# Performance work log

Measured on AMD Instinct MI355X. Metric: run time of the kernel, lower is better.

The kernel has to match this reference:

```python
import jax, jax.numpy as jnp
import numpy as np


def fwht(x):
    """Unnormalized fast Walsh-Hadamard transform over a 1-D vector (len = power of 2).
    Matches the torch chunk/cat stage ordering (MSB-first butterfly)."""
    n = x.shape[0]
    ll = int(round(np.log2(n)))
    for ii in range(ll):
        x = x.reshape(2 ** ii, 2, -1)
        x = jnp.concatenate([x[:, :1] + x[:, 1:], x[:, :1] - x[:, 1:]], axis=1)
    return x.reshape(n)


@jax.custom_vjp
def fwht_ff(x):
    # mirrors torch FastWalshHadamard.apply: plain FWHT forward,
    # backward = FWHT(grad) / sqrt(n) (as defined in the original autograd Function)
    return fwht(x)

def _fwht_ff_fwd(x):
    scale = jnp.asarray(1.0 / np.sqrt(float(x.shape[0])), x.dtype)
    return fwht(x), scale

def _fwht_ff_bwd(scale, g):
    return (scale * fwht(g),)

fwht_ff.defvjp(_fwht_ff_fwd, _fwht_ff_bwd)


def fastfood(theta, BB, Pi, GG, DD):
    """Fastfood projection of theta (dim dd) to DD dims using fixed vars."""
    LL = BB.shape[0]
    dd = theta.shape[0]
    k = min(dd, LL)  # F.pad with negative pad truncates; replicate that
    xx = jnp.zeros(LL, theta.dtype).at[:k].set(theta[:k])
    m2 = fwht(BB * xx)          # H B x
    m4 = m2[Pi] * GG            # G Pi H B x
    m5 = fwht_ff(m4)            # H G Pi H B x
    divisor = jnp.sqrt(LL * jnp.sum(GG * GG))
    return m5[:DD] / (divisor * np.sqrt(float(DD) / LL))


def _mk_ff_vars(key, DD):
    ll = int(np.ceil(np.log2(DD)))
    LL = 2 ** ll
    k1, k2, k3 = jax.random.split(key, 3)
    BB = jax.random.randint(k1, (LL,), 0, 2).astype(jnp.float32) * 2.0 - 1.0
    Pi = jax.random.permutation(k2, LL).astype(jnp.int32)
    GG = jax.random.normal(k3, (LL,), dtype=jnp.float32)
    return BB, Pi, GG


D_IN, D_HID, D_OUT = 768, 3072, 768
INTRINSIC = 2048
BATCH = 256


def setup_inputs() -> dict:
    key = jax.random.key(0)
    ks = jax.random.split(key, 12)
    x = jax.random.normal(ks[0], (BATCH, D_IN), dtype=jnp.float32)
    # original initializes intrinsic_parameter to zeros; use small randn so the
    # Fastfood path contributes non-trivially to the output for testing
    theta = jax.random.normal(ks[1], (INTRINSIC,), dtype=jnp.float32) * 0.01
    init_W1 = jax.random.normal(ks[2], (D_HID, D_IN), dtype=jnp.float32) * 0.02
    init_b1 = jax.random.normal(ks[3], (D_HID,), dtype=jnp.float32) * 0.02
    init_W2 = jax.random.normal(ks[4], (D_OUT, D_HID), dtype=jnp.float32) * 0.02
    init_b2 = jax.random.normal(ks[5], (D_OUT,), dtype=jnp.float32) * 0.02
    BB_W1, Pi_W1, GG_W1 = _mk_ff_vars(ks[6], D_HID * D_IN)
    BB_b1, Pi_b1, GG_b1 = _mk_ff_vars(ks[7], D_HID)
    BB_W2, Pi_W2, GG_W2 = _mk_ff_vars(ks[8], D_OUT * D_HID)
    BB_b2, Pi_b2, GG_b2 = _mk_ff_vars(ks[9], D_OUT)
    return {
        'x': x, 'theta': theta,
        'init_W1': init_W1, 'init_b1': init_b1, 'init_W2': init_W2, 'init_b2': init_b2,
        'BB_W1': BB_W1, 'Pi_W1': Pi_W1, 'GG_W1': GG_W1,
        'BB_b1': BB_b1, 'Pi_b1': Pi_b1, 'GG_b1': GG_b1,
        'BB_W2': BB_W2, 'Pi_W2': Pi_W2, 'GG_W2': GG_W2,
        'BB_b2': BB_b2, 'Pi_b2': Pi_b2, 'GG_b2': GG_b2,
    }


def reference(x, theta, init_W1, init_b1, init_W2, init_b2,
              BB_W1, Pi_W1, GG_W1, BB_b1, Pi_b1, GG_b1,
              BB_W2, Pi_W2, GG_W2, BB_b2, Pi_b2, GG_b2):
    # param = initial_value + fastfood(theta) for every wrapped parameter
    W1 = init_W1 + fastfood(theta, BB_W1, Pi_W1, GG_W1, init_W1.size).reshape(init_W1.shape)
    b1 = init_b1 + fastfood(theta, BB_b1, Pi_b1, GG_b1, init_b1.size)
    W2 = init_W2 + fastfood(theta, BB_W2, Pi_W2, GG_W2, init_W2.size).reshape(init_W2.shape)
    b2 = init_b2 + fastfood(theta, BB_b2, Pi_b2, GG_b2, init_b2.size)
    # wrapped module forward: Linear -> ReLU -> Linear
    h = jax.nn.relu(x @ W1.T + b1)
    return h @ W2.T + b2
```

## Files before the change

### kernel.cpp

```cpp
#include <hip/hip_runtime.h>
#include <hip/hip_bf16.h>

typedef __attribute__((ext_vector_type(8))) short bf16x8;
typedef __attribute__((ext_vector_type(8))) unsigned short u16x8;
typedef __attribute__((ext_vector_type(4))) float f32x4;

template <int N, int S>
__device__ __forceinline__ void reg_fwht(float* v) {
#pragma unroll
  for (int h = 1; h < N; h <<= 1)
#pragma unroll
    for (int g = 0; g < N; g += 2 * h)
#pragma unroll
      for (int j = 0; j < h; ++j) {
        float a = v[(g + j) * S], b = v[(g + j + h) * S];
        v[(g + j) * S] = a + b;
        v[(g + j + h) * S] = a - b;
      }
}

__device__ __forceinline__ unsigned short f2bf(float f) {
  unsigned u = __float_as_uint(f);
  unsigned r = (u + 0x7fff + ((u >> 16) & 1)) >> 16;
  return (unsigned short)r;
}

__device__ __forceinline__ void lds_fwht(float* s, int n, int tid, int T) {
  for (int h = 1; h < n; h <<= 1) {
    __syncthreads();
    for (int t = tid; t < (n >> 1); t += T) {
      int i0 = ((t & ~(h - 1)) << 1) | (t & (h - 1));
      int i1 = i0 + h;
      float a = s[i0], b = s[i1];
      s[i0] = a + b;
      s[i1] = a - b;
    }
  }
  __syncthreads();
}

__device__ __forceinline__ void fwht2048_block(float w[8], float* pad,
                                               float* dst, int t) {
  reg_fwht<8, 1>(w);
#pragma unroll
  for (int j = 0; j < 8; ++j) {
    int i = t + 256 * j;
    pad[i + 4 * (i >> 5)] = w[j];
  }
  __syncthreads();
  {
    int base = 8 * t + 4 * (t >> 2);
    float4 a = *(float4*)(pad + base);
    float4 b = *(float4*)(pad + base + 4);
    float u[8] = {a.x, a.y, a.z, a.w, b.x, b.y, b.z, b.w};
    reg_fwht<8, 1>(u);
    *(float4*)(pad + base) = make_float4(u[0], u[1], u[2], u[3]);
    *(float4*)(pad + base + 4) = make_float4(u[4], u[5], u[6], u[7]);
  }
  __syncthreads();
  {
    int b0 = (t & 7) + 64 * (t >> 3);
    float u[8];
#pragma unroll
    for (int j = 0; j < 8; ++j) {
      int i = b0 + 8 * j;
      u[j] = pad[i + 4 * (i >> 5)];
    }
    reg_fwht<8, 1>(u);
#pragma unroll
    for (int j = 0; j < 8; ++j) {
      int i = b0 + 8 * j;
      pad[i + 4 * (i >> 5)] = u[j];
    }
  }
  __syncthreads();
#pragma unroll
  for (int g = 0; g < 2; ++g) {
    int b0 = (t & 63) + 256 * ((g << 2) | (t >> 6));
    float u[4];
#pragma unroll
    for (int j = 0; j < 4; ++j) {
      int i = b0 + 64 * j;
      u[j] = pad[i + 4 * (i >> 5)];
    }
    reg_fwht<4, 1>(u);
#pragma unroll
    for (int j = 0; j < 4; ++j) dst[b0 + 64 * j] = u[j];
  }
  __syncthreads();
}

__global__ __launch_bounds__(256) void k_pre(
    const float* __restrict__ theta, const float* __restrict__ BB0,
    const float* __restrict__ BB1, float* __restrict__ m2s,
    const float* __restrict__ x, __hip_bfloat16* __restrict__ xb) {
  __shared__ __align__(16) float pad[2304];
  int b = blockIdx.x, t = threadIdx.x;
  if (b < 2) {
    const float* BB = b ? BB1 : BB0;
    float w[8];
#pragma unroll
    for (int j = 0; j < 8; ++j) {
      int i = t + 256 * j;
      w[j] = BB[i] * theta[i];
    }
    fwht2048_block(w, pad, m2s + b * 2048, t);
  } else {
    int id0 = (b - 2) * 256 + t;
#pragma unroll
    for (int it = 0; it < 2; ++it) {
      int id = id0 + it * 24576;
      float4 xv = ((const float4*)x)[id];
      ushort4 o;
      o.x = f2bf(xv.x);
      o.y = f2bf(xv.y);
      o.z = f2bf(xv.z);
      o.w = f2bf(xv.w);
      ((ushort4*)xb)[id] = o;
    }
  }
}

#define LLW 4194304

__global__ __launch_bounds__(256) void k_front(
    const int* __restrict__ Pi1, const float* __restrict__ GG1,
    const int* __restrict__ Pi2, const float* __restrict__ GG2,
    const float* __restrict__ m2s, unsigned short* __restrict__ m4b,
    float* __restrict__ partial, const float* __restrict__ theta,
    const float* __restrict__ BBb1, const int* __restrict__ Pib1,
    const float* __restrict__ GGb1, const float* __restrict__ ib1,
    float* __restrict__ b1w, const float* __restrict__ BBb2,
    const int* __restrict__ Pib2, const float* __restrict__ GGb2,
    const float* __restrict__ ib2, float* __restrict__ b2w) {
  __shared__ __align__(16) float s[9216];
  __shared__ float red[4];
  int b = blockIdx.x, t = threadIdx.x;

  if (b >= 2) {
    int bb = b - 2;
    int pipe = bb >> 9, chunk = bb & 511;
    const int* Pi = pipe ? Pi2 : Pi1;
    const float* GG = pipe ? GG2 : GG1;
    const float* mm = m2s + pipe * 2048;
    for (int u = t; u < 512; u += 256) ((float4*)s)[u] = ((const float4*)mm)[u];
    __syncthreads();

    long base = (long)chunk * 8192;
    const int4* p4 = (const int4*)(Pi + base);
    const float4* g4 = (const float4*)(GG + base);
    float v[32];
    float lsum = 0.f;
#pragma unroll
    for (int j = 0; j < 8; ++j) {
      int4 p = p4[t + j * 256];
      float4 g = g4[t + j * 256];
      lsum += g.x * g.x + g.y * g.y + g.z * g.z + g.w * g.w;
      v[j * 4 + 0] = s[p.x & 2047] * g.x;
      v[j * 4 + 1] = s[p.y & 2047] * g.y;
      v[j * 4 + 2] = s[p.z & 2047] * g.z;
      v[j * 4 + 3] = s[p.w & 2047] * g.w;
    }
    for (int off = 32; off; off >>= 1) lsum += __shfl_down(lsum, off, 64);
    if ((t & 63) == 0) red[t >> 6] = lsum;

#pragma unroll
    for (int e = 0; e < 4; ++e) reg_fwht<8, 4>(v + e);

    __syncthreads();
    if (t == 0) partial[pipe * 512 + chunk] = red[0] + red[1] + red[2] + red[3];

#pragma unroll
    for (int j = 0; j < 8; ++j) {
      int A = t * 4 + 4 * (t >> 3) + j * 1152;
      *(float4*)(s + A) =
          make_float4(v[j * 4], v[j * 4 + 1], v[j * 4 + 2], v[j * 4 + 3]);
    }
    __syncthreads();
    {
      int b0 = (t & 31) + (t >> 5) * 1024;
      float w[32];
#pragma unroll
      for (int j2 = 0; j2 < 32; ++j2) {
        int i = b0 + j2 * 32;
        w[j2] = s[i + 4 * (i >> 5)];
      }
      reg_fwht<32, 1>(w);
#pragma unroll
      for (int j2 = 0; j2 < 32; ++j2) {
        int i = b0 + j2 * 32;
        s[i + 4 * (i >> 5)] = w[j2];
      }
    }
    __syncthreads();
#pragma unroll
    for (int q = 0; q < 8; ++q) {
      float4 r = *(const float4*)(s + t * 36 + q * 4);
      v[q * 4 + 0] = r.x;
      v[q * 4 + 1] = r.y;
      v[q * 4 + 2] = r.z;
      v[q * 4 + 3] = r.w;
    }
    reg_fwht<32, 1>(v);
    unsigned short* o = m4b + (long)pipe * LLW;
    long a0 = (long)(2 * t) * 8192 + (long)chunk * 16;
#pragma unroll
    for (int q = 0; q < 4; ++q) {
      u16x8 pk;
#pragma unroll
      for (int e = 0; e < 8; ++e) pk[e] = f2bf(v[q * 8 + e]);
      *(u16x8*)(o + a0 + (q >> 1) * 8192 + (q & 1) * 8) = pk;
    }
  } else if (b == 0) {
    float* tabd = s + 6144;
    float w[8];
#pragma unroll
    for (int j = 0; j < 8; ++j) {
      int i = t + 256 * j;
      w[j] = BBb1[i] * theta[i];
    }
    fwht2048_block(w, s, tabd, t);

    float w16[16];
    float lsum = 0.f;
#pragma unroll
    for (int j = 0; j < 16; ++j) {
      int i = t + 256 * j;
      float g = GGb1[i];
      lsum += g * g;
      w16[j] = tabd[Pib1[i] & 2047] * g;
    }
    reg_fwht<16, 1>(w16);
#pragma unroll
    for (int j = 0; j < 16; ++j) {
      int i = t + 256 * j;
      s[i + 4 * (i >> 5)] = w16[j];
    }
    for (int off = 32; off; off >>= 1) lsum += __shfl_down(lsum, off, 64);
    if ((t & 63) == 0) s[4608 + (t >> 6)] = lsum;
    __syncthreads();
    float S = s[4608] + s[4609] + s[4610] + s[4611];
    {
      int base16 = 16 * t + 4 * (t >> 1);
      float u[16];
#pragma unroll
      for (int q = 0; q < 4; ++q) {
        float4 r = *(float4*)(s + base16 + q * 4);
        u[q * 4 + 0] = r.x;
        u[q * 4 + 1] = r.y;
        u[q * 4 + 2] = r.z;
        u[q * 4 + 3] = r.w;
      }
      reg_fwht<16, 1>(u);
#pragma unroll
      for (int q = 0; q < 4; ++q)
        *(float4*)(s + base16 + q * 4) =
            make_float4(u[q * 4], u[q * 4 + 1], u[q * 4 + 2], u[q * 4 + 3]);
    }
    __syncthreads();
    {
      float scale = 1.0f / sqrtf(S * 3072.0f);
      int b0 = (t & 15) + 256 * (t >> 4);
      float u[16];
#pragma unroll
      for (int j = 0; j < 16; ++j) {
        int i = b0 + 16 * j;
        u[j] = s[i + 4 * (i >> 5)];
      }
      reg_fwht<16, 1>(u);
#pragma unroll
      for (int j = 0; j < 16; ++j) {
        int i = b0 + 16 * j;
        if (i < 3072) b1w[i] = ib1[i] + u[j] * scale;
      }
    }
  } else {
    float* tab2 = s;
    float* m42 = s + 1024;
    for (int i = t; i < 1024; i += 256) tab2[i] = BBb2[i] * theta[i];
    lds_fwht(tab2, 1024, t, 256);
    float lsum = 0.f;
    for (int i = t; i < 1024; i += 256) {
      float g = GGb2[i];
      lsum += g * g;
      m42[i] = tab2[Pib2[i] & 1023] * g;
    }
    for (int off = 32; off; off >>= 1) lsum += __shfl_down(lsum, off, 64);
    if ((t & 63) == 0) s[2048 + (t >> 6)] = lsum;
    lds_fwht(m42, 1024, t, 256);
    float S = s[2048] + s[2049] + s[2050] + s[2051];
    float scale = 1.0f / sqrtf(S * 768.0f);
    for (int i = t; i < 768; i += 256) b2w[i] = ib2[i] + m42[i] * scale;
  }
}

__global__ __launch_bounds__(256) void k_f2c(
    const unsigned short* __restrict__ m4b, const float* __restrict__ iW1,
    const float* __restrict__ iW2, const float* __restrict__ partial,
    __hip_bfloat16* __restrict__ W1b, __hip_bfloat16* __restrict__ W2b) {
  __shared__ __align__(16) float s[10480];
  __shared__ float red[4];
  int b = blockIdx.x, t = threadIdx.x;
  int pipe = b >> 9;
  int lb = b & 511;
  int g = ((lb & 7) << 6) | (lb >> 3);
  int l0 = g * 16;
  const unsigned short* mp = m4b + (long)pipe * LLW + (long)g * 8192;
  const float* initW = pipe ? iW2 : iW1;
  unsigned short* outW = (unsigned short*)(pipe ? W2b : W1b);

  {
    float ps = partial[pipe * 512 + t] + partial[pipe * 512 + 256 + t];
    for (int off = 32; off; off >>= 1) ps += __shfl_down(ps, off, 64);
    if ((t & 63) == 0) red[t >> 6] = ps;
  }

#pragma unroll
  for (int q = 0; q < 4; ++q) {
    u16x8 raw = *(const u16x8*)(mp + t * 32 + q * 8);
    int r = 2 * t + (q >> 1), cb = (q & 1) * 8;
    float* dp = s + r * 20 + (r >> 5) * 16 + cb;
    float4 f0, f1v;
    f0.x = __uint_as_float((unsigned)raw[0] << 16);
    f0.y = __uint_as_float((unsigned)raw[1] << 16);
    f0.z = __uint_as_float((unsigned)raw[2] << 16);
    f0.w = __uint_as_float((unsigned)raw[3] << 16);
    f1v.x = __uint_as_float((unsigned)raw[4] << 16);
    f1v.y = __uint_as_float((unsigned)raw[5] << 16);
    f1v.z = __uint_as_float((unsigned)raw[6] << 16);
    f1v.w = __uint_as_float((unsigned)raw[7] << 16);
    *(float4*)dp = f0;
    *(float4*)(dp + 4) = f1v;
  }
  __syncthreads();

  {
    int c = t & 15, rg = t >> 4;
    float w[32];
#pragma unroll
    for (int j = 0; j < 32; ++j) {
      int r = rg * 32 + j;
      w[j] = s[r * 20 + (r >> 5) * 16 + c];
    }
    reg_fwht<32, 1>(w);
#pragma unroll
    for (int j = 0; j < 32; ++j) {
      int r = rg * 32 + j;
      s[r * 20 + (r >> 5) * 16 + c] = w[j];
    }
  }
  __syncthreads();

  {
    int c = t & 15;
    float w[32];
#pragma unroll
    for (int k = 0; k < 2; ++k) {
      int b0 = (t >> 4) * 2 + k;
#pragma unroll
      for (int j4 = 0; j4 < 16; ++j4) {
        int r = b0 + 32 * j4;
        w[k * 16 + j4] = s[r * 20 + (r >> 5) * 16 + c];
      }
      reg_fwht<16, 1>(w + k * 16);
#pragma unroll
      for (int j4 = 0; j4 < 16; ++j4) {
        int r = b0 + 32 * j4;
        s[r * 20 + (r >> 5) * 16 + c] = w[k * 16 + j4];
      }
    }
  }
  __syncthreads();

  float S = red[0] + red[1] + red[2] + red[3];
  float scale = 1.0f / sqrtf(S * 2359296.0f);
#pragma unroll
  for (int u = 0; u < 5; ++u) {
    int idx = t + u * 256;
    if (idx < 1152) {
      int r = idx >> 2, c4 = (idx & 3) * 4;
      const float* sp = s + r * 20 + (r >> 5) * 16 + c4;
      long gi = (long)r * 8192 + l0 + c4;
      float4 iv = *(const float4*)(initW + gi);
      ushort4 pk;
      pk.x = f2bf(iv.x + sp[0] * scale);
      pk.y = f2bf(iv.y + sp[1] * scale);
      pk.z = f2bf(iv.z + sp[2] * scale);
      pk.w = f2bf(iv.w + sp[3] * scale);
      *(ushort4*)(outW + gi) = pk;
    }
  }
}

template <int NACC, int SPLITK, bool RELU, bool OUT_BF16>
__global__ __launch_bounds__(256) void k_gemm(
    const __hip_bfloat16* __restrict__ A, const __hip_bfloat16* __restrict__ B,
    const float* __restrict__ bias, void* __restrict__ C, int M, int N, int K) {
  __shared__ float red[4 * NACC * 320];
  int wave = threadIdx.x >> 6, lane = threadIdx.x & 63;
  int tileid = blockIdx.x * (4 / SPLITK) + wave / SPLITK;
  int sk = wave % SPLITK;
  int ntiles = N / (16 * NACC);
  int mt = tileid / ntiles, nt = tileid % ntiles;
  int ml = lane & 15;
  int q = lane >> 4;
  const short* As = (const short*)A;
  const short* Bs = (const short*)B;
  long arow = (long)(mt * 16 + ml) * K + q * 8;
  int KS = K / SPLITK, k0 = sk * KS;
  f32x4 acc[NACC] = {};
  for (int k = k0; k < k0 + KS; k += 32) {
    bf16x8 av = *(const bf16x8*)(As + arow + k);
#pragma unroll
    for (int a = 0; a < NACC; ++a) {
      int n = nt * 16 * NACC + a * 16 + ml;
      bf16x8 bv = *(const bf16x8*)(Bs + (long)n * K + q * 8 + k);
      acc[a] = __builtin_amdgcn_mfma_f32_16x16x32_bf16(av, bv, acc[a], 0, 0, 0);
    }
  }
#pragma unroll
  for (int a = 0; a < NACC; ++a)
#pragma unroll
    for (int r = 0; r < 4; ++r)
      red[(wave * NACC + a) * 320 + lane * 5 + r] = acc[a][r];
  __syncthreads();
  if (sk == 0) {
#pragma unroll
    for (int a = 0; a < NACC; ++a) {
      int n = nt * 16 * NACC + a * 16 + ml;
      float bv = bias[n];
#pragma unroll
      for (int r = 0; r < 4; ++r) {
        float vv = bv;
#pragma unroll
        for (int j = 0; j < SPLITK; ++j)
          vv += red[((wave + j) * NACC + a) * 320 + lane * 5 + r];
        int mm = mt * 16 + q * 4 + r;
        if (RELU) vv = fmaxf(vv, 0.f);
        if (OUT_BF16)
          ((__hip_bfloat16*)C)[(long)mm * N + n] = __float2bfloat16(vv);
        else
          ((float*)C)[(long)mm * N + n] = vv;
      }
    }
  }
}

#define OFF_PART 0
#define OFF_M2S 4096
#define OFF_M4B (OFF_M2S + 16384)
#define OFF_W1B (OFF_M4B + 2 * LLW * 2)
#define OFF_W2B (OFF_W1B + 4718592)
#define OFF_HB (OFF_W2B + 4718592)
#define OFF_XB (OFF_HB + 1572864)
#define OFF_B1 (OFF_XB + 393216)
#define OFF_B2 (OFF_B1 + 12288)

extern "C" void kernel_launch(void* const* d_in, const int* in_sizes, int n_in,
                              void* d_out, int out_size, void* d_ws,
                              size_t ws_size, hipStream_t stream) {
  const float* x = (const float*)d_in[0];
  const float* theta = (const float*)d_in[1];
  const float* iW1 = (const float*)d_in[2];
  const float* ib1 = (const float*)d_in[3];
  const float* iW2 = (const float*)d_in[4];
  const float* ib2 = (const float*)d_in[5];
  const float* BB_W1 = (const float*)d_in[6];
  const int* Pi_W1 = (const int*)d_in[7];
  const float* GG_W1 = (const float*)d_in[8];
  const float* BB_b1 = (const float*)d_in[9];
  const int* Pi_b1 = (const int*)d_in[10];
  const float* GG_b1 = (const float*)d_in[11];
  const float* BB_W2 = (const float*)d_in[12];
  const int* Pi_W2 = (const int*)d_in[13];
  const float* GG_W2 = (const float*)d_in[14];
  const float* BB_b2 = (const float*)d_in[15];
  const int* Pi_b2 = (const int*)d_in[16];
  const float* GG_b2 = (const float*)d_in[17];

  char* ws = (char*)d_ws;
  float* partial = (float*)(ws + OFF_PART);
  float* m2s = (float*)(ws + OFF_M2S);
  unsigned short* m4b = (unsigned short*)(ws + OFF_M4B);
  __hip_bfloat16* W1b = (__hip_bfloat16*)(ws + OFF_W1B);
  __hip_bfloat16* W2b = (__hip_bfloat16*)(ws + OFF_W2B);
  __hip_bfloat16* hb = (__hip_bfloat16*)(ws + OFF_HB);
  __hip_bfloat16* xb = (__hip_bfloat16*)(ws + OFF_XB);
  float* b1w = (float*)(ws + OFF_B1);
  float* b2w = (float*)(ws + OFF_B2);

  k_pre<<<98, 256, 0, stream>>>(theta, BB_W1, BB_W2, m2s, x, xb);
  k_front<<<1026, 256, 0, stream>>>(Pi_W1, GG_W1, Pi_W2, GG_W2, m2s, m4b,
                                    partial, theta, BB_b1, Pi_b1, GG_b1, ib1,
                                    b1w, BB_b2, Pi_b2, GG_b2, ib2, b2w);
  k_f2c<<<1024, 256, 0, stream>>>(m4b, iW1, iW2, partial, W1b, W2b);
  k_gemm<2, 2, true, true><<<768, 256, 0, stream>>>(xb, W1b, b1w, hb, 256,
                                                    3072, 768);
  k_gemm<1, 4, false, false><<<768, 256, 0, stream>>>(hb, W2b, b2w, d_out, 256,
                                                      768, 3072);
}
```

Measured before the change: 217.8 us.

## Fuse prelude into front kernel and overlap W2 conversion with first GEMM

Each front block now recomputes the 2048-point H·B·theta transform itself instead of reading it from a separate pre-kernel, and the x→bf16 conversion moves into extra blocks of the same launch. The f2c kernel is split so W1 is built first, then a mixed kernel runs the W2 conversion alongside the first GEMM. This removes one launch and one global round trip and lets memory-bound and MFMA work share the GPU. The cost is redundant FWHT work in all 1024 blocks and possible load imbalance between heterogeneous blocks. The mixed kernel also uses the 10480-float f2c shared array for the GEMM reduction buffer.

```diff
diff --git a/kernel.cpp b/kernel.cpp
--- a/kernel.cpp
+++ b/kernel.cpp
@@ -90,23 +90,187 @@
   __syncthreads();
 }
 
-__global__ __launch_bounds__(256) void k_pre(
-    const float* __restrict__ theta, const float* __restrict__ BB0,
-    const float* __restrict__ BB1, float* __restrict__ m2s,
-    const float* __restrict__ x, __hip_bfloat16* __restrict__ xb) {
-  __shared__ __align__(16) float pad[2304];
+#define LLW 4194304
+
+__global__ __launch_bounds__(256) void k_front(
+    const float* __restrict__ BB1, const int* __restrict__ Pi1,
+    const float* __restrict__ GG1, const float* __restrict__ BB2,
+    const int* __restrict__ Pi2, const float* __restrict__ GG2,
+    unsigned short* __restrict__ m4b, float* __restrict__ partial,
+    const float* __restrict__ theta, const float* __restrict__ BBb1,
+    const int* __restrict__ Pib1, const float* __restrict__ GGb1,
+    const float* __restrict__ ib1, float* __restrict__ b1w,
+    const float* __restrict__ BBb2, const int* __restrict__ Pib2,
+    const float* __restrict__ GGb2, const float* __restrict__ ib2,
+    float* __restrict__ b2w, const float* __restrict__ x,
+    __hip_bfloat16* __restrict__ xb) {
+  __shared__ __align__(16) float s[9216];
+  __shared__ float red[4];
   int b = blockIdx.x, t = threadIdx.x;
-  if (b < 2) {
-    const float* BB = b ? BB1 : BB0;
+
+  if (b < 1024) {
+    int pipe = b >> 9, chunk = b & 511;
+    const float* BB = pipe ? BB2 : BB1;
+    const int* Pi = pipe ? Pi2 : Pi1;
+    const float* GG = pipe ? GG2 : GG1;
+
+    {
+      float w8[8];
+#pragma unroll
+      for (int j = 0; j < 8; ++j) {
+        int i = t + 256 * j;
+        w8[j] = BB[i] * theta[i];
+      }
+      fwht2048_block(w8, s + 2304, s, t);
+    }
+
+    long base = (long)chunk * 8192;
+    const int4* p4 = (const int4*)(Pi + base);
+    const float4* g4 = (const float4*)(GG + base);
+    float v[32];
+    float lsum = 0.f;
+#pragma unroll
+    for (int j = 0; j < 8; ++j) {
+      int4 p = p4[t + j * 256];
+      float4 g = g4[t + j * 256];
+      lsum += g.x * g.x + g.y * g.y + g.z * g.z + g.w * g.w;
+      v[j * 4 + 0] = s[p.x & 2047] * g.x;
+      v[j * 4 + 1] = s[p.y & 2047] * g.y;
+      v[j * 4 + 2] = s[p.z & 2047] * g.z;
+      v[j * 4 + 3] = s[p.w & 2047] * g.w;
+    }
+    for (int off = 32; off; off >>= 1) lsum += __shfl_down(lsum, off, 64);
+    if ((t & 63) == 0) red[t >> 6] = lsum;
+
+#pragma unroll
+    for (int e = 0; e < 4; ++e) reg_fwht<8, 4>(v + e);
+
+    __syncthreads();
+    if (t == 0) partial[pipe * 512 + chunk] = red[0] + red[1] + red[2] + red[3];
+
+#pragma unroll
+    for (int j = 0; j < 8; ++j) {
+      int A = t * 4 + 4 * (t >> 3) + j * 1152;
+      *(float4*)(s + A) =
+          make_float4(v[j * 4], v[j * 4 + 1], v[j * 4 + 2], v[j * 4 + 3]);
+    }
+    __syncthreads();
+    {
+      int b0 = (t & 31) + (t >> 5) * 1024;
+      float w[32];
+#pragma unroll
+      for (int j2 = 0; j2 < 32; ++j2) {
+        int i = b0 + j2 * 32;
+        w[j2] = s[i + 4 * (i >> 5)];
+      }
+      reg_fwht<32, 1>(w);
+#pragma unroll
+      for (int j2 = 0; j2 < 32; ++j2) {
+        int i = b0 + j2 * 32;
+        s[i + 4 * (i >> 5)] = w[j2];
+      }
+    }
+    __syncthreads();
+#pragma unroll
+    for (int q = 0; q < 8; ++q) {
+      float4 r = *(const float4*)(s + t * 36 + q * 4);
+      v[q * 4 + 0] = r.x;
+      v[q * 4 + 1] = r.y;
+      v[q * 4 + 2] = r.z;
+      v[q * 4 + 3] = r.w;
+    }
+    reg_fwht<32, 1>(v);
+    unsigned short* o = m4b + (long)pipe * LLW;
+    long a0 = (long)(2 * t) * 8192 + (long)chunk * 16;
+#pragma unroll
+    for (int q = 0; q < 4; ++q) {
+      u16x8 pk;
+#pragma unroll
+      for (int e = 0; e < 8; ++e) pk[e] = f2bf(v[q * 8 + e]);
+      *(u16x8*)(o + a0 + (q >> 1) * 8192 + (q & 1) * 8) = pk;
+    }
+  } else if (b == 1024) {
+    float* tabd = s + 6144;
     float w[8];
 #pragma unroll
     for (int j = 0; j < 8; ++j) {
       int i = t + 256 * j;
-      w[j] = BB[i] * theta[i];
-    }
-    fwht2048_block(w, pad, m2s + b * 2048, t);
+      w[j] = BBb1[i] * theta[i];
+    }
+    fwht2048_block(w, s, tabd, t);
+
+    float w16[16];
+    float lsum = 0.f;
+#pragma unroll
+    for (int j = 0; j < 16; ++j) {
+      int i = t + 256 * j;
+      float g = GGb1[i];
+      lsum += g * g;
+      w16[j] = tabd[Pib1[i] & 2047] * g;
+    }
+    reg_fwht<16, 1>(w16);
+#pragma unroll
+    for (int j = 0; j < 16; ++j) {
+      int i = t + 256 * j;
+      s[i + 4 * (i >> 5)] = w16[j];
+    }
+    for (int off = 32; off; off >>= 1) lsum += __shfl_down(lsum, off, 64);
+    if ((t & 63) == 0) s[4608 + (t >> 6)] = lsum;
+    __syncthreads();
+    float S = s[4608] + s[4609] + s[4610] + s[4611];
+    {
+      int base16 = 16 * t + 4 * (t >> 1);
+      float u[16];
+#pragma unroll
+      for (int q = 0; q < 4; ++q) {
+        float4 r = *(float4*)(s + base16 + q * 4);
+        u[q * 4 + 0] = r.x;
+        u[q * 4 + 1] = r.y;
+        u[q * 4 + 2] = r.z;
+        u[q * 4 + 3] = r.w;
+      }
+      reg_fwht<16, 1>(u);
+#pragma unroll
+      for (int q = 0; q < 4; ++q)
+        *(float4*)(s + base16 + q * 4) =
+            make_float4(u[q * 4], u[q * 4 + 1], u[q * 4 + 2], u[q * 4 + 3]);
+    }
+    __syncthreads();
+    {
+      float scale = 1.0f / sqrtf(S * 3072.0f);
+      int b0 = (t & 15) + 256 * (t >> 4);
+      float u[16];
+#pragma unroll
+      for (int j = 0; j < 16; ++j) {
+        int i = b0 + 16 * j;
+        u[j] = s[i + 4 * (i >> 5)];
+      }
+      reg_fwht<16, 1>(u);
+#pragma unroll
+      for (int j = 0; j < 16; ++j) {
+        int i = b0 + 16 * j;
+        if (i < 3072) b1w[i] = ib1[i] + u[j] * scale;
+      }
+    }
+  } else if (b == 1025) {
+    float* tab2 = s;
+    float* m42 = s + 1024;
+    for (int i = t; i < 1024; i += 256) tab2[i] = BBb2[i] * theta[i];
+    lds_fwht(tab2, 1024, t, 256);
+    float lsum = 0.f;
+    for (int i = t; i < 1024; i += 256) {
+      float g = GGb2[i];
+      lsum += g * g;
+      m42[i] = tab2[Pib2[i] & 1023] * g;
+    }
+    for (int off = 32; off; off >>= 1) lsum += __shfl_down(lsum, off, 64);
+    if ((t & 63) == 0) s[2048 + (t >> 6)] = lsum;
+    lds_fwht(m42, 1024, t, 256);
+    float S = s[2048] + s[2049] + s[2050] + s[2051];
+    float scale = 1.0f / sqrtf(S * 768.0f);
+    for (int i = t; i < 768; i += 256) b2w[i] = ib2[i] + m42[i] * scale;
   } else {
-    int id0 = (b - 2) * 256 + t;
+    int id0 = (b - 1026) * 256 + t;
 #pragma unroll
     for (int it = 0; it < 2; ++it) {
       int id = id0 + it * 24576;
@@ -121,196 +285,17 @@
   }
 }
 
-#define LLW 4194304
-
-__global__ __launch_bounds__(256) void k_front(
-    const int* __restrict__ Pi1, const float* __restrict__ GG1,
-    const int* __restrict__ Pi2, const float* __restrict__ GG2,
-    const float* __restrict__ m2s, unsigned short* __restrict__ m4b,
-    float* __restrict__ partial, const float* __restrict__ theta,
-    const float* __restrict__ BBb1, const int* __restrict__ Pib1,
-    const float* __restrict__ GGb1, const float* __restrict__ ib1,
-    float* __restrict__ b1w, const float* __restrict__ BBb2,
-    const int* __restrict__ Pib2, const float* __restrict__ GGb2,
-    const float* __restrict__ ib2, float* __restrict__ b2w) {
-  __shared__ __align__(16) float s[9216];
-  __shared__ float red[4];
-  int b = blockIdx.x, t = threadIdx.x;
-
-  if (b >= 2) {
-    int bb = b - 2;
-    int pipe = bb >> 9, chunk = bb & 511;
-    const int* Pi = pipe ? Pi2 : Pi1;
-    const float* GG = pipe ? GG2 : GG1;
-    const float* mm = m2s + pipe * 2048;
-    for (int u = t; u < 512; u += 256) ((float4*)s)[u] = ((const float4*)mm)[u];
-    __syncthreads();
-
-    long base = (long)chunk * 8192;
-    const int4* p4 = (const int4*)(Pi + base);
-    const float4* g4 = (const float4*)(GG + base);
-    float v[32];
-    float lsum = 0.f;
-#pragma unroll
-    for (int j = 0; j < 8; ++j) {
-      int4 p = p4[t + j * 256];
-      float4 g = g4[t + j * 256];
-      lsum += g.x * g.x + g.y * g.y + g.z * g.z + g.w * g.w;
-      v[j * 4 + 0] = s[p.x & 2047] * g.x;
-      v[j * 4 + 1] = s[p.y & 2047] * g.y;
-      v[j * 4 + 2] = s[p.z & 2047] * g.z;
-      v[j * 4 + 3] = s[p.w & 2047] * g.w;
-    }
-    for (int off = 32; off; off >>= 1) lsum += __shfl_down(lsum, off, 64);
-    if ((t & 63) == 0) red[t >> 6] = lsum;
-
-#pragma unroll
-    for (int e = 0; e < 4; ++e) reg_fwht<8, 4>(v + e);
-
-    __syncthreads();
-    if (t == 0) partial[pipe * 512 + chunk] = red[0] + red[1] + red[2] + red[3];
-
-#pragma unroll
-    for (int j = 0; j < 8; ++j) {
-      int A = t * 4 + 4 * (t >> 3) + j * 1152;
-      *(float4*)(s + A) =
-          make_float4(v[j * 4], v[j * 4 + 1], v[j * 4 + 2], v[j * 4 + 3]);
-    }
-    __syncthreads();
-    {
-      int b0 = (t & 31) + (t >> 5) * 1024;
-      float w[32];
-#pragma unroll
-      for (int j2 = 0; j2 < 32; ++j2) {
-        int i = b0 + j2 * 32;
-        w[j2] = s[i + 4 * (i >> 5)];
-      }
-      reg_fwht<32, 1>(w);
-#pragma unroll
-      for (int j2 = 0; j2 < 32; ++j2) {
-        int i = b0 + j2 * 32;
-        s[i + 4 * (i >> 5)] = w[j2];
-      }
-    }
-    __syncthreads();
-#pragma unroll
-    for (int q = 0; q < 8; ++q) {
-      float4 r = *(const float4*)(s + t * 36 + q * 4);
-      v[q * 4 + 0] = r.x;
-      v[q * 4 + 1] = r.y;
-      v[q * 4 + 2] = r.z;
-      v[q * 4 + 3] = r.w;
-    }
-    reg_fwht<32, 1>(v);
-    unsigned short* o = m4b + (long)pipe * LLW;
-    long a0 = (long)(2 * t) * 8192 + (long)chunk * 16;
-#pragma unroll
-    for (int q = 0; q < 4; ++q) {
-      u16x8 pk;
-#pragma unroll
-      for (int e = 0; e < 8; ++e) pk[e] = f2bf(v[q * 8 + e]);
-      *(u16x8*)(o + a0 + (q >> 1) * 8192 + (q & 1) * 8) = pk;
-    }
-  } else if (b == 0) {
-    float* tabd = s + 6144;
-    float w[8];
-#pragma unroll
-    for (int j = 0; j < 8; ++j) {
-      int i = t + 256 * j;
-      w[j] = BBb1[i] * theta[i];
-    }
-    fwht2048_block(w, s, tabd, t);
-
-    float w16[16];
-    float lsum = 0.f;
-#pragma unroll
-    for (int j = 0; j < 16; ++j) {
-      int i = t + 256 * j;
-      float g = GGb1[i];
-      lsum += g * g;
-      w16[j] = tabd[Pib1[i] & 2047] * g;
-    }
-    reg_fwht<16, 1>(w16);
-#pragma unroll
-    for (int j = 0; j < 16; ++j) {
-      int i = t + 256 * j;
-      s[i + 4 * (i >> 5)] = w16[j];
-    }
-    for (int off = 32; off; off >>= 1) lsum += __shfl_down(lsum, off, 64);
-    if ((t & 63) == 0) s[4608 + (t >> 6)] = lsum;
-    __syncthreads();
-    float S = s[4608] + s[4609] + s[4610] + s[4611];
-    {
-      int base16 = 16 * t + 4 * (t >> 1);
-      float u[16];
-#pragma unroll
-      for (int q = 0; q < 4; ++q) {
-        float4 r = *(float4*)(s + base16 + q * 4);
-        u[q * 4 + 0] = r.x;
-        u[q * 4 + 1] = r.y;
-        u[q * 4 + 2] = r.z;
-        u[q * 4 + 3] = r.w;
-      }
-      reg_fwht<16, 1>(u);
-#pragma unroll
-      for (int q = 0; q < 4; ++q)
-        *(float4*)(s + base16 + q * 4) =
-            make_float4(u[q * 4], u[q * 4 + 1], u[q * 4 + 2], u[q * 4 + 3]);
-    }
-    __syncthreads();
-    {
-      float scale = 1.0f / sqrtf(S * 3072.0f);
-      int b0 = (t & 15) + 256 * (t >> 4);
-      float u[16];
-#pragma unroll
-      for (int j = 0; j < 16; ++j) {
-        int i = b0 + 16 * j;
-        u[j] = s[i + 4 * (i >> 5)];
-      }
-      reg_fwht<16, 1>(u);
-#pragma unroll
-      for (int j = 0; j < 16; ++j) {
-        int i = b0 + 16 * j;
-        if (i < 3072) b1w[i] = ib1[i] + u[j] * scale;
-      }
-    }
-  } else {
-    float* tab2 = s;
-    float* m42 = s + 1024;
-    for (int i = t; i < 1024; i += 256) tab2[i] = BBb2[i] * theta[i];
-    lds_fwht(tab2, 1024, t, 256);
-    float lsum = 0.f;
-    for (int i = t; i < 1024; i += 256) {
-      float g = GGb2[i];
-      lsum += g * g;
-      m42[i] = tab2[Pib2[i] & 1023] * g;
-    }
-    for (int off = 32; off; off >>= 1) lsum += __shfl_down(lsum, off, 64);
-    if ((t & 63) == 0) s[2048 + (t >> 6)] = lsum;
-    lds_fwht(m42, 1024, t, 256);
-    float S = s[2048] + s[2049] + s[2050] + s[2051];
-    float scale = 1.0f / sqrtf(S * 768.0f);
-    for (int i = t; i < 768; i += 256) b2w[i] = ib2[i] + m42[i] * scale;
-  }
-}
-
-__global__ __launch_bounds__(256) void k_f2c(
-    const unsigned short* __restrict__ m4b, const float* __restrict__ iW1,
-    const float* __restrict__ iW2, const float* __restrict__ partial,
-    __hip_bfloat16* __restrict__ W1b, __hip_bfloat16* __restrict__ W2b) {
-  __shared__ __align__(16) float s[10480];
-  __shared__ float red[4];
-  int b = blockIdx.x, t = threadIdx.x;
-  int pipe = b >> 9;
-  int lb = b & 511;
+__device__ __forceinline__ void f2c_body(const unsigned short* __restrict__ mpipe,
+                                         const float* __restrict__ initW,
+                                         unsigned short* __restrict__ outW,
+                                         const float* __restrict__ partial_p,
+                                         int lb, int t, float* s, float* red) {
   int g = ((lb & 7) << 6) | (lb >> 3);
   int l0 = g * 16;
-  const unsigned short* mp = m4b + (long)pipe * LLW + (long)g * 8192;
-  const float* initW = pipe ? iW2 : iW1;
-  unsigned short* outW = (unsigned short*)(pipe ? W2b : W1b);
+  const unsigned short* mp = mpipe + (long)g * 8192;
 
   {
-    float ps = partial[pipe * 512 + t] + partial[pipe * 512 + 256 + t];
+    float ps = partial_p[t] + partial_p[256 + t];
     for (int off = 32; off; off >>= 1) ps += __shfl_down(ps, off, 64);
     if ((t & 63) == 0) red[t >> 6] = ps;
   }
@@ -393,12 +378,12 @@
 }
 
 template <int NACC, int SPLITK, bool RELU, bool OUT_BF16>
-__global__ __launch_bounds__(256) void k_gemm(
+__device__ __forceinline__ void gemm_body(
     const __hip_bfloat16* __restrict__ A, const __hip_bfloat16* __restrict__ B,
-    const float* __restrict__ bias, void* __restrict__ C, int M, int N, int K) {
-  __shared__ float red[4 * NACC * 320];
-  int wave = threadIdx.x >> 6, lane = threadIdx.x & 63;
-  int tileid = blockIdx.x * (4 / SPLITK) + wave / SPLITK;
+    const float* __restrict__ bias, void* __restrict__ C, int M, int N, int K,
+    int bid, int tid, float* red) {
+  int wave = tid >> 6, lane = tid & 63;
+  int tileid = bid * (4 / SPLITK) + wave / SPLITK;
   int sk = wave % SPLITK;
   int ntiles = N / (16 * NACC);
   int mt = tileid / ntiles, nt = tileid % ntiles;
@@ -444,6 +429,41 @@
       }
     }
   }
+}
+
+__global__ __launch_bounds__(256) void k_f2c_a(
+    const unsigned short* __restrict__ m4b, const float* __restrict__ iW1,
+    const float* __restrict__ partial, __hip_bfloat16* __restrict__ W1b) {
+  __shared__ __align__(16) float s[10480];
+  __shared__ float red[4];
+  f2c_body(m4b, iW1, (unsigned short*)W1b, partial, blockIdx.x, threadIdx.x, s,
+           red);
+}
+
+__global__ __launch_bounds__(256) void k_mix(
+    const unsigned short* __restrict__ m4b, const float* __restrict__ iW2,
+    const float* __restrict__ partial, __hip_bfloat16* __restrict__ W2b,
+    const __hip_bfloat16* __restrict__ xb, const __hip_bfloat16* __restrict__ W1b,
+    const float* __restrict__ b1w, __hip_bfloat16* __restrict__ hb) {
+  __shared__ __align__(16) float s[10480];
+  __shared__ float red[4];
+  int b = blockIdx.x, t = threadIdx.x;
+  if (b < 512) {
+    f2c_body(m4b + (long)LLW, iW2, (unsigned short*)W2b, partial + 512, b, t,
+             s, red);
+  } else {
+    gemm_body<2, 2, true, true>(xb, W1b, b1w, hb, 256, 3072, 768, b - 512, t,
+                                s);
+  }
+}
+
+template <int NACC, int SPLITK, bool RELU, bool OUT_BF16>
+__global__ __launch_bounds__(256) void k_gemm(
+    const __hip_bfloat16* __restrict__ A, const __hip_bfloat16* __restrict__ B,
+    const float* __restrict__ bias, void* __restrict__ C, int M, int N, int K) {
+  __shared__ float red[4 * NACC * 320];
+  gemm_body<NACC, SPLITK, RELU, OUT_BF16>(A, B, bias, C, M, N, K, blockIdx.x,
+                                          threadIdx.x, red);
 }
 
 #define OFF_PART 0
@@ -480,7 +500,6 @@
 
   char* ws = (char*)d_ws;
   float* partial = (float*)(ws + OFF_PART);
-  float* m2s = (float*)(ws + OFF_M2S);
   unsigned short* m4b = (unsigned short*)(ws + OFF_M4B);
   __hip_bfloat16* W1b = (__hip_bfloat16*)(ws + OFF_W1B);
   __hip_bfloat16* W2b = (__hip_bfloat16*)(ws + OFF_W2B);
@@ -489,13 +508,12 @@
   float* b1w = (float*)(ws + OFF_B1);
   float* b2w = (float*)(ws + OFF_B2);
 
-  k_pre<<<98, 256, 0, stream>>>(theta, BB_W1, BB_W2, m2s, x, xb);
-  k_front<<<1026, 256, 0, stream>>>(Pi_W1, GG_W1, Pi_W2, GG_W2, m2s, m4b,
-                                    partial, theta, BB_b1, Pi_b1, GG_b1, ib1,
-                                    b1w, BB_b2, Pi_b2, GG_b2, ib2, b2w);
-  k_f2c<<<1024, 256, 0, stream>>>(m4b, iW1, iW2, partial, W1b, W2b);
-  k_gemm<2, 2, true, true><<<768, 256, 0, stream>>>(xb, W1b, b1w, hb, 256,
-                                                    3072, 768);
+  k_front<<<1122, 256, 0, stream>>>(BB_W1, Pi_W1, GG_W1, BB_W2, Pi_W2, GG_W2,
+                                    m4b, partial, theta, BB_b1, Pi_b1, GG_b1,
+                                    ib1, b1w, BB_b2, Pi_b2, GG_b2, ib2, b2w, x,
+                                    xb);
+  k_f2c_a<<<512, 256, 0, stream>>>(m4b, iW1, partial, W1b);
+  k_mix<<<1280, 256, 0, stream>>>(m4b, iW2, partial, W2b, xb, W1b, b1w, hb);
   k_gemm<1, 4, false, false><<<768, 256, 0, stream>>>(hb, W2b, b2w, d_out, 256,
                                                       768, 3072);
 }
```

After: 218.1 us. No clear change (+0.1%).

## Fuse pre-FWHT into front kernel and enlarge GEMM tiles

Applied to the files above, without the earlier changes.

Removes the separate k_pre launch by having each of the 1024 chunk blocks redundantly compute the 2048-point H·B·theta transform in shared memory, and moves the x-to-bf16 conversion into extra blocks of k_front. This drops one kernel launch and the m2s round trip through global memory, at the cost of repeating the small FWHT in every block. The GEMM template parameters are also doubled so each block does more work and half as many blocks are launched.

```diff
diff --git a/kernel.cpp b/kernel.cpp
--- a/kernel.cpp
+++ b/kernel.cpp
@@ -4,6 +4,8 @@
 typedef __attribute__((ext_vector_type(8))) short bf16x8;
 typedef __attribute__((ext_vector_type(8))) unsigned short u16x8;
 typedef __attribute__((ext_vector_type(4))) float f32x4;
+
+#define LLW 4194304
 
 template <int N, int S>
 __device__ __forceinline__ void reg_fwht(float* v) {
@@ -90,23 +92,186 @@
   __syncthreads();
 }
 
-__global__ __launch_bounds__(256) void k_pre(
-    const float* __restrict__ theta, const float* __restrict__ BB0,
-    const float* __restrict__ BB1, float* __restrict__ m2s,
-    const float* __restrict__ x, __hip_bfloat16* __restrict__ xb) {
-  __shared__ __align__(16) float pad[2304];
+__global__ __launch_bounds__(256) void k_front(
+    const float* __restrict__ BB1, const int* __restrict__ Pi1,
+    const float* __restrict__ GG1, const float* __restrict__ BB2,
+    const int* __restrict__ Pi2, const float* __restrict__ GG2,
+    unsigned short* __restrict__ m4b, float* __restrict__ partial,
+    const float* __restrict__ theta, const float* __restrict__ BBb1,
+    const int* __restrict__ Pib1, const float* __restrict__ GGb1,
+    const float* __restrict__ ib1, float* __restrict__ b1w,
+    const float* __restrict__ BBb2, const int* __restrict__ Pib2,
+    const float* __restrict__ GGb2, const float* __restrict__ ib2,
+    float* __restrict__ b2w, const float* __restrict__ x,
+    __hip_bfloat16* __restrict__ xb) {
+  __shared__ __align__(16) float s[9216];
+  __shared__ float red[4];
   int b = blockIdx.x, t = threadIdx.x;
-  if (b < 2) {
-    const float* BB = b ? BB1 : BB0;
+
+  if (b >= 2 && b < 1026) {
+    int bb = b - 2;
+    int pipe = bb >> 9, chunk = bb & 511;
+    const float* BB = pipe ? BB2 : BB1;
+    const int* Pi = pipe ? Pi2 : Pi1;
+    const float* GG = pipe ? GG2 : GG1;
+
+    {
+      float w8[8];
+#pragma unroll
+      for (int j = 0; j < 8; ++j) {
+        int i = t + 256 * j;
+        w8[j] = BB[i] * theta[i];
+      }
+      fwht2048_block(w8, s + 2304, s, t);
+    }
+
+    long base = (long)chunk * 8192;
+    const int4* p4 = (const int4*)(Pi + base);
+    const float4* g4 = (const float4*)(GG + base);
+    float v[32];
+    float lsum = 0.f;
+#pragma unroll
+    for (int j = 0; j < 8; ++j) {
+      int4 pp = p4[t + j * 256];
+      float4 g = g4[t + j * 256];
+      lsum += g.x * g.x + g.y * g.y + g.z * g.z + g.w * g.w;
+      v[j * 4 + 0] = s[pp.x & 2047] * g.x;
+      v[j * 4 + 1] = s[pp.y & 2047] * g.y;
+      v[j * 4 + 2] = s[pp.z & 2047] * g.z;
+      v[j * 4 + 3] = s[pp.w & 2047] * g.w;
+    }
+    for (int off = 32; off; off >>= 1) lsum += __shfl_down(lsum, off, 64);
+    if ((t & 63) == 0) red[t >> 6] = lsum;
+
+#pragma unroll
+    for (int e = 0; e < 4; ++e) reg_fwht<8, 4>(v + e);
+
+    __syncthreads();
+    if (t == 0) partial[pipe * 512 + chunk] = red[0] + red[1] + red[2] + red[3];
+
+#pragma unroll
+    for (int j = 0; j < 8; ++j) {
+      int A = t * 4 + 4 * (t >> 3) + j * 1152;
+      *(float4*)(s + A) =
+          make_float4(v[j * 4], v[j * 4 + 1], v[j * 4 + 2], v[j * 4 + 3]);
+    }
+    __syncthreads();
+    {
+      int b0 = (t & 31) + (t >> 5) * 1024;
+      float w[32];
+#pragma unroll
+      for (int j2 = 0; j2 < 32; ++j2) {
+        int i = b0 + j2 * 32;
+        w[j2] = s[i + 4 * (i >> 5)];
+      }
+      reg_fwht<32, 1>(w);
+#pragma unroll
+      for (int j2 = 0; j2 < 32; ++j2) {
+        int i = b0 + j2 * 32;
+        s[i + 4 * (i >> 5)] = w[j2];
+      }
+    }
+    __syncthreads();
+#pragma unroll
+    for (int q = 0; q < 8; ++q) {
+      float4 r = *(const float4*)(s + t * 36 + q * 4);
+      v[q * 4 + 0] = r.x;
+      v[q * 4 + 1] = r.y;
+      v[q * 4 + 2] = r.z;
+      v[q * 4 + 3] = r.w;
+    }
+    reg_fwht<32, 1>(v);
+    unsigned short* o = m4b + (long)pipe * LLW;
+    long a0 = (long)(2 * t) * 8192 + (long)chunk * 16;
+#pragma unroll
+    for (int q = 0; q < 4; ++q) {
+      u16x8 pk;
+#pragma unroll
+      for (int e = 0; e < 8; ++e) pk[e] = f2bf(v[q * 8 + e]);
+      *(u16x8*)(o + a0 + (q >> 1) * 8192 + (q & 1) * 8) = pk;
+    }
+  } else if (b == 0) {
+    float* tabd = s + 6144;
     float w[8];
 #pragma unroll
     for (int j = 0; j < 8; ++j) {
       int i = t + 256 * j;
-      w[j] = BB[i] * theta[i];
-    }
-    fwht2048_block(w, pad, m2s + b * 2048, t);
+      w[j] = BBb1[i] * theta[i];
+    }
+    fwht2048_block(w, s, tabd, t);
+
+    float w16[16];
+    float lsum = 0.f;
+#pragma unroll
+    for (int j = 0; j < 16; ++j) {
+      int i = t + 256 * j;
+      float g = GGb1[i];
+      lsum += g * g;
+      w16[j] = tabd[Pib1[i] & 2047] * g;
+    }
+    reg_fwht<16, 1>(w16);
+#pragma unroll
+    for (int j = 0; j < 16; ++j) {
+      int i = t + 256 * j;
+      s[i + 4 * (i >> 5)] = w16[j];
+    }
+    for (int off = 32; off; off >>= 1) lsum += __shfl_down(lsum, off, 64);
+    if ((t & 63) == 0) s[4608 + (t >> 6)] = lsum;
+    __syncthreads();
+    float S = s[4608] + s[4609] + s[4610] + s[4611];
+    {
+      int base16 = 16 * t + 4 * (t >> 1);
+      float u[16];
+#pragma unroll
+      for (int q = 0; q < 4; ++q) {
+        float4 r = *(float4*)(s + base16 + q * 4);
+        u[q * 4 + 0] = r.x;
+        u[q * 4 + 1] = r.y;
+        u[q * 4 + 2] = r.z;
+        u[q * 4 + 3] = r.w;
+      }
+      reg_fwht<16, 1>(u);
+#pragma unroll
+      for (int q = 0; q < 4; ++q)
+        *(float4*)(s + base16 + q * 4) =
+            make_float4(u[q * 4], u[q * 4 + 1], u[q * 4 + 2], u[q * 4 + 3]);
+    }
+    __syncthreads();
+    {
+      float scale = 1.0f / sqrtf(S * 3072.0f);
+      int b0 = (t & 15) + 256 * (t >> 4);
+      float u[16];
+#pragma unroll
+      for (int j = 0; j < 16; ++j) {
+        int i = b0 + 16 * j;
+        u[j] = s[i + 4 * (i >> 5)];
+      }
+      reg_fwht<16, 1>(u);
+#pragma unroll
+      for (int j = 0; j < 16; ++j) {
+        int i = b0 + 16 * j;
+        if (i < 3072) b1w[i] = ib1[i] + u[j] * scale;
+      }
+    }
+  } else if (b == 1) {
+    float* tab2 = s;
+    float* m42 = s + 1024;
+    for (int i = t; i < 1024; i += 256) tab2[i] = BBb2[i] * theta[i];
+    lds_fwht(tab2, 1024, t, 256);
+    float lsum = 0.f;
+    for (int i = t; i < 1024; i += 256) {
+      float g = GGb2[i];
+      lsum += g * g;
+      m42[i] = tab2[Pib2[i] & 1023] * g;
+    }
+    for (int off = 32; off; off >>= 1) lsum += __shfl_down(lsum, off, 64);
+    if ((t & 63) == 0) s[2048 + (t >> 6)] = lsum;
+    lds_fwht(m42, 1024, t, 256);
+    float S = s[2048] + s[2049] + s[2050] + s[2051];
+    float scale = 1.0f / sqrtf(S * 768.0f);
+    for (int i = t; i < 768; i += 256) b2w[i] = ib2[i] + m42[i] * scale;
   } else {
-    int id0 = (b - 2) * 256 + t;
+    int id0 = (b - 1026) * 256 + t;
 #pragma unroll
     for (int it = 0; it < 2; ++it) {
       int id = id0 + it * 24576;
@@ -118,179 +283,6 @@
       o.w = f2bf(xv.w);
       ((ushort4*)xb)[id] = o;
     }
-  }
-}
-
-#define LLW 4194304
-
-__global__ __launch_bounds__(256) void k_front(
-    const int* __restrict__ Pi1, const float* __restrict__ GG1,
-    const int* __restrict__ Pi2, const float* __restrict__ GG2,
-    const float* __restrict__ m2s, unsigned short* __restrict__ m4b,
-    float* __restrict__ partial, const float* __restrict__ theta,
-    const float* __restrict__ BBb1, const int* __restrict__ Pib1,
-    const float* __restrict__ GGb1, const float* __restrict__ ib1,
-    float* __restrict__ b1w, const float* __restrict__ BBb2,
-    const int* __restrict__ Pib2, const float* __restrict__ GGb2,
-    const float* __restrict__ ib2, float* __restrict__ b2w) {
-  __shared__ __align__(16) float s[9216];
-  __shared__ float red[4];
-  int b = blockIdx.x, t = threadIdx.x;
-
-  if (b >= 2) {
-    int bb = b - 2;
-    int pipe = bb >> 9, chunk = bb & 511;
-    const int* Pi = pipe ? Pi2 : Pi1;
-    const float* GG = pipe ? GG2 : GG1;
-    const float* mm = m2s + pipe * 2048;
-    for (int u = t; u < 512; u += 256) ((float4*)s)[u] = ((const float4*)mm)[u];
-    __syncthreads();
-
-    long base = (long)chunk * 8192;
-    const int4* p4 = (const int4*)(Pi + base);
-    const float4* g4 = (const float4*)(GG + base);
-    float v[32];
-    float lsum = 0.f;
-#pragma unroll
-    for (int j = 0; j < 8; ++j) {
-      int4 p = p4[t + j * 256];
-      float4 g = g4[t + j * 256];
-      lsum += g.x * g.x + g.y * g.y + g.z * g.z + g.w * g.w;
-      v[j * 4 + 0] = s[p.x & 2047] * g.x;
-      v[j * 4 + 1] = s[p.y & 2047] * g.y;
-      v[j * 4 + 2] = s[p.z & 2047] * g.z;
-      v[j * 4 + 3] = s[p.w & 2047] * g.w;
-    }
-    for (int off = 32; off; off >>= 1) lsum += __shfl_down(lsum, off, 64);
-    if ((t & 63) == 0) red[t >> 6] = lsum;
-
-#pragma unroll
-    for (int e = 0; e < 4; ++e) reg_fwht<8, 4>(v + e);
-
-    __syncthreads();
-    if (t == 0) partial[pipe * 512 + chunk] = red[0] + red[1] + red[2] + red[3];
-
-#pragma unroll
-    for (int j = 0; j < 8; ++j) {
-      int A = t * 4 + 4 * (t >> 3) + j * 1152;
-      *(float4*)(s + A) =
-          make_float4(v[j * 4], v[j * 4 + 1], v[j * 4 + 2], v[j * 4 + 3]);
-    }
-    __syncthreads();
-    {
-      int b0 = (t & 31) + (t >> 5) * 1024;
-      float w[32];
-#pragma unroll
-      for (int j2 = 0; j2 < 32; ++j2) {
-        int i = b0 + j2 * 32;
-        w[j2] = s[i + 4 * (i >> 5)];
-      }
-      reg_fwht<32, 1>(w);
-#pragma unroll
-      for (int j2 = 0; j2 < 32; ++j2) {
-        int i = b0 + j2 * 32;
-        s[i + 4 * (i >> 5)] = w[j2];
-      }
-    }
-    __syncthreads();
-#pragma unroll
-    for (int q = 0; q < 8; ++q) {
-      float4 r = *(const float4*)(s + t * 36 + q * 4);
-      v[q * 4 + 0] = r.x;
-      v[q * 4 + 1] = r.y;
-      v[q * 4 + 2] = r.z;
-      v[q * 4 + 3] = r.w;
-    }
-    reg_fwht<32, 1>(v);
-    unsigned short* o = m4b + (long)pipe * LLW;
-    long a0 = (long)(2 * t) * 8192 + (long)chunk * 16;
-#pragma unroll
-    for (int q = 0; q < 4; ++q) {
-      u16x8 pk;
-#pragma unroll
-      for (int e = 0; e < 8; ++e) pk[e] = f2bf(v[q * 8 + e]);
-      *(u16x8*)(o + a0 + (q >> 1) * 8192 + (q & 1) * 8) = pk;
-    }
-  } else if (b == 0) {
-    float* tabd = s + 6144;
-    float w[8];
-#pragma unroll
-    for (int j = 0; j < 8; ++j) {
-      int i = t + 256 * j;
-      w[j] = BBb1[i] * theta[i];
-    }
-    fwht2048_block(w, s, tabd, t);
-
-    float w16[16];
-    float lsum = 0.f;
-#pragma unroll
-    for (int j = 0; j < 16; ++j) {
-      int i = t + 256 * j;
-      float g = GGb1[i];
-      lsum += g * g;
-      w16[j] = tabd[Pib1[i] & 2047] * g;
-    }
-    reg_fwht<16, 1>(w16);
-#pragma unroll
-    for (int j = 0; j < 16; ++j) {
-      int i = t + 256 * j;
-      s[i + 4 * (i >> 5)] = w16[j];
-    }
-    for (int off = 32; off; off >>= 1) lsum += __shfl_down(lsum, off, 64);
-    if ((t & 63) == 0) s[4608 + (t >> 6)] = lsum;
-    __syncthreads();
-    float S = s[4608] + s[4609] + s[4610] + s[4611];
-    {
-      int base16 = 16 * t + 4 * (t >> 1);
-      float u[16];
-#pragma unroll
-      for (int q = 0; q < 4; ++q) {
-        float4 r = *(float4*)(s + base16 + q * 4);
-        u[q * 4 + 0] = r.x;
-        u[q * 4 + 1] = r.y;
-        u[q * 4 + 2] = r.z;
-        u[q * 4 + 3] = r.w;
-      }
-      reg_fwht<16, 1>(u);
-#pragma unroll
-      for (int q = 0; q < 4; ++q)
-        *(float4*)(s + base16 + q * 4) =
-            make_float4(u[q * 4], u[q * 4 + 1], u[q * 4 + 2], u[q * 4 + 3]);
-    }
-    __syncthreads();
-    {
-      float scale = 1.0f / sqrtf(S * 3072.0f);
-      int b0 = (t & 15) + 256 * (t >> 4);
-      float u[16];
-#pragma unroll
-      for (int j = 0; j < 16; ++j) {
-        int i = b0 + 16 * j;
-        u[j] = s[i + 4 * (i >> 5)];
-      }
-      reg_fwht<16, 1>(u);
-#pragma unroll
-      for (int j = 0; j < 16; ++j) {
-        int i = b0 + 16 * j;
-        if (i < 3072) b1w[i] = ib1[i] + u[j] * scale;
-      }
-    }
-  } else {
-    float* tab2 = s;
-    float* m42 = s + 1024;
-    for (int i = t; i < 1024; i += 256) tab2[i] = BBb2[i] * theta[i];
-    lds_fwht(tab2, 1024, t, 256);
-    float lsum = 0.f;
-    for (int i = t; i < 1024; i += 256) {
-      float g = GGb2[i];
-      lsum += g * g;
-      m42[i] = tab2[Pib2[i] & 1023] * g;
-    }
-    for (int off = 32; off; off >>= 1) lsum += __shfl_down(lsum, off, 64);
-    if ((t & 63) == 0) s[2048 + (t >> 6)] = lsum;
-    lds_fwht(m42, 1024, t, 256);
-    float S = s[2048] + s[2049] + s[2050] + s[2051];
-    float scale = 1.0f / sqrtf(S * 768.0f);
-    for (int i = t; i < 768; i += 256) b2w[i] = ib2[i] + m42[i] * scale;
   }
 }
 
@@ -480,7 +472,6 @@
 
   char* ws = (char*)d_ws;
   float* partial = (float*)(ws + OFF_PART);
-  float* m2s = (float*)(ws + OFF_M2S);
   unsigned short* m4b = (unsigned short*)(ws + OFF_M4B);
   __hip_bfloat16* W1b = (__hip_bfloat16*)(ws + OFF_W1B);
   __hip_bfloat16* W2b = (__hip_bfloat16*)(ws + OFF_W2B);
@@ -489,13 +480,13 @@
   float* b1w = (float*)(ws + OFF_B1);
   float* b2w = (float*)(ws + OFF_B2);
 
-  k_pre<<<98, 256, 0, stream>>>(theta, BB_W1, BB_W2, m2s, x, xb);
-  k_front<<<1026, 256, 0, stream>>>(Pi_W1, GG_W1, Pi_W2, GG_W2, m2s, m4b,
-                                    partial, theta, BB_b1, Pi_b1, GG_b1, ib1,
-                                    b1w, BB_b2, Pi_b2, GG_b2, ib2, b2w);
+  k_front<<<1122, 256, 0, stream>>>(BB_W1, Pi_W1, GG_W1, BB_W2, Pi_W2, GG_W2,
+                                    m4b, partial, theta, BB_b1, Pi_b1, GG_b1,
+                                    ib1, b1w, BB_b2, Pi_b2, GG_b2, ib2, b2w, x,
+                                    xb);
   k_f2c<<<1024, 256, 0, stream>>>(m4b, iW1, iW2, partial, W1b, W2b);
-  k_gemm<2, 2, true, true><<<768, 256, 0, stream>>>(xb, W1b, b1w, hb, 256,
+  k_gemm<4, 2, true, true><<<384, 256, 0, stream>>>(xb, W1b, b1w, hb, 256,
                                                     3072, 768);
-  k_gemm<1, 4, false, false><<<768, 256, 0, stream>>>(hb, W2b, b2w, d_out, 256,
+  k_gemm<2, 4, false, false><<<384, 256, 0, stream>>>(hb, W2b, b2w, d_out, 256,
                                                       768, 3072);
 }
```

New measurement: 219.3 us. No clear change (+0.7%).
